# Optimization experiments

Measured on AMD Instinct MI355X. Metric: run time of the kernel, lower is better.

Reference implementation:

```python
import jax, jax.numpy as jnp
import numpy as np

V, E, U, B, L, H = 32000, 256, 1024, 64, 2048, 1024  # vocab, embed, dec_units, batch, enc_len, enc_hidden


def setup_inputs() -> dict:
    key = jax.random.key(0)
    ks = jax.random.split(key, 14)
    s = 0.02
    return {
        "x": jax.random.randint(ks[0], (B, 1), 0, V),
        "hidden": jax.random.normal(ks[1], (B, U), jnp.float32),
        "enc_output": jax.random.normal(ks[2], (B, L, H), jnp.float32),
        "emb": jax.random.normal(ks[3], (V, E), jnp.float32) * s,
        "w1": jax.random.normal(ks[4], (H, U), jnp.float32) * s,
        "b1": jnp.zeros((U,), jnp.float32),
        "w2": jax.random.normal(ks[5], (U, U), jnp.float32) * s,
        "b2": jnp.zeros((U,), jnp.float32),
        "v_w": jax.random.normal(ks[6], (U, 1), jnp.float32) * s,
        "v_b": jnp.zeros((1,), jnp.float32),
        "gru_k": jax.random.normal(ks[7], (H + E, 3 * U), jnp.float32) * s,
        "gru_rk": jax.random.normal(ks[8], (U, 3 * U), jnp.float32) * s,
        "gru_b": jnp.zeros((3 * U,), jnp.float32),
        "out_w": jax.random.normal(ks[9], (U, V), jnp.float32) * s,
        "out_b": jnp.zeros((V,), jnp.float32),
    }


def reference(x, hidden, enc_output, emb, w1, b1, w2, b2, v_w, v_b,
              gru_k, gru_rk, gru_b, out_w, out_b):
    # ---- Bahdanau additive attention ----
    # score: [B, L, 1]
    hid_t = (hidden @ w2 + b2)[:, None, :]                      # [B,1,U]
    score = jnp.tanh(enc_output @ w1 + b1 + hid_t) @ v_w + v_b  # [B,L,1]
    attention_weights = jax.nn.softmax(score, axis=1)           # softmax over seq axis
    context = jnp.sum(attention_weights * enc_output, axis=1)   # [B,H]

    # ---- embed current token and concat [context, embedded] ----
    xe = emb[x[:, 0]]                                           # [B,E]
    xin = jnp.concatenate([context, xe], axis=-1)               # [B,H+E]

    # ---- single GRU step; original calls gru(x) w/o initial_state -> h0 = 0 ----
    # Keras gate order [z, r, h], reset_after=False
    h0 = jnp.zeros((xin.shape[0], U), xin.dtype)
    zi = xin @ gru_k + gru_b                                    # [B,3U]
    z = jax.nn.sigmoid(zi[:, :U] + h0 @ gru_rk[:, :U])
    r = jax.nn.sigmoid(zi[:, U:2 * U] + h0 @ gru_rk[:, U:2 * U])
    hh = jnp.tanh(zi[:, 2 * U:] + (r * h0) @ gru_rk[:, 2 * U:])
    state = z * h0 + (1.0 - z) * hh                             # [B,U]

    # ---- output projection ----
    logits = state @ out_w + out_b                              # [B,V]
    return logits, state, attention_weights
```

## Files before the change

### kernel.cpp

```cpp
#include <hip/hip_runtime.h>
#include <hip/hip_bf16.h>
#include <stdint.h>

#define Bz 64
#define Lz 2048
#define Hz 1024
#define Uz 1024
#define Vz 32000
#define Ez 256

typedef __attribute__((ext_vector_type(8))) short bf16x8;
typedef __attribute__((ext_vector_type(4))) float f32x4;

__device__ __forceinline__ unsigned short f2bf(float f) {
    unsigned int u = __float_as_uint(f);
    u += 0x7fffu + ((u >> 16) & 1u);
    return (unsigned short)(u >> 16);
}

__device__ __forceinline__ float tanh_fast(float x) {
    float e = __expf(2.0f * x);
    return (e - 1.0f) * __builtin_amdgcn_rcpf(e + 1.0f);
}

__device__ __forceinline__ void async_cp16(const void* g, void* l) {
    __builtin_amdgcn_global_load_lds(
        (const __attribute__((address_space(1))) void*)g,
        (__attribute__((address_space(3))) void*)l, 16, 0, 0);
}

__global__ void pack_w1_kernel(const float* __restrict__ w1,
                               unsigned short* __restrict__ w1p) {
    __shared__ float tile[32][257];
    int nb = blockIdx.x;
    int kb = blockIdx.y;
    int t  = threadIdx.x;
#pragma unroll
    for (int i = 0; i < 32; ++i)
        tile[i][t] = w1[(size_t)(kb * 32 + i) * Uz + nb * 256 + t];
    __syncthreads();
    union { uint4 v[4]; unsigned short s[32]; } u;
#pragma unroll
    for (int kk = 0; kk < 32; ++kk) u.s[kk] = f2bf(tile[kk][t]);
    uint4* d4 = (uint4*)(w1p + (size_t)kb * 32768 + (size_t)(nb * 256 + t) * 32);
#pragma unroll
    for (int j = 0; j < 4; ++j) d4[j] = u.v[j];
}

__global__ void transpose_hidden_kernel(const float* __restrict__ hidden,
                                        float* __restrict__ hT) {
    __shared__ float tile[64][65];
    int cb = blockIdx.x;
    int t  = threadIdx.x;
    int tc = t & 63, tr = t >> 6;
#pragma unroll
    for (int i = 0; i < 16; ++i) {
        int r = i * 4 + tr;
        tile[r][tc] = hidden[(size_t)r * Uz + cb * 64 + tc];
    }
    __syncthreads();
#pragma unroll
    for (int i = 0; i < 16; ++i) {
        int k = i * 4 + tr;
        hT[(size_t)(cb * 64 + k) * 64 + tc] = tile[tc][k];
    }
}

__global__ __launch_bounds__(256)
void hid_gemm_kernel(const float* __restrict__ hT, const float* __restrict__ w2,
                     float* __restrict__ hid) {
    int col = blockIdx.x * 256 + threadIdx.x;
    int k0  = blockIdx.y * 64;
    float acc[64];
#pragma unroll
    for (int r = 0; r < 64; ++r) acc[r] = 0.f;
#pragma unroll 4
    for (int k = 0; k < 64; ++k) {
        float w = w2[(size_t)(k0 + k) * Uz + col];
        const float* srow = hT + (size_t)(k0 + k) * 64;
#pragma unroll
        for (int r = 0; r < 64; ++r) acc[r] = fmaf(srow[r], w, acc[r]);
    }
#pragma unroll
    for (int r = 0; r < 64; ++r) atomicAdd(&hid[(size_t)r * Uz + col], acc[r]);
}

__global__ __launch_bounds__(256, 2)
void score_kernel(const float* __restrict__ enc,
                  const unsigned short* __restrict__ w1p,
                  const float* __restrict__ b1, const float* __restrict__ b2,
                  const float* __restrict__ hid, const float* __restrict__ vw,
                  float* __restrict__ scores) {
    __shared__ __align__(16) float lA[64 * 32];
    __shared__ __align__(16) unsigned short lB[512 * 32];

    const int t    = threadIdx.x;
    const int lane = t & 63;
    const int wave = t >> 6;
    const int ln   = lane & 15;
    const int q    = lane >> 4;
    const int n0   = blockIdx.x * 512;
    const int m0   = blockIdx.y * 64;
    const int bidx = m0 >> 11;

    f32x4 acc[4][8];
    const f32x4 zero = {0.f, 0.f, 0.f, 0.f};
#pragma unroll
    for (int ms = 0; ms < 4; ++ms)
#pragma unroll
        for (int s = 0; s < 8; ++s) acc[ms][s] = zero;

    const char* w1base = ((const char*)w1p) + n0 * 64;

    for (int kt = 0; kt < 32; ++kt) {
        __syncthreads();
        const char* bsrc = w1base + kt * 65536;
#pragma unroll
        for (int i = 0; i < 8; ++i) {
            int cb = i * 256 + t;
            async_cp16(bsrc + cb * 16, ((char*)lB) + cb * 16);
        }
#pragma unroll
        for (int i = 0; i < 2; ++i) {
            int P = i * 256 + t;
            int m = P >> 3, p = P & 7;
            int c = p ^ (m & 7);
            async_cp16(enc + (size_t)(m0 + m) * Hz + kt * 32 + c * 4,
                       ((char*)lA) + P * 16);
        }
        __syncthreads();

        bf16x8 afr[4];
#pragma unroll
        for (int ms = 0; ms < 4; ++ms) {
            int m = ms * 16 + ln;
            int c0 = (2 * q) ^ (m & 7);
            int c1 = (2 * q + 1) ^ (m & 7);
            float4 x0 = *(const float4*)&lA[m * 32 + c0 * 4];
            float4 x1 = *(const float4*)&lA[m * 32 + c1 * 4];
            union { bf16x8 v; __hip_bfloat162 h[4]; } u;
            u.h[0] = __float22bfloat162_rn(make_float2(x0.x, x0.y));
            u.h[1] = __float22bfloat162_rn(make_float2(x0.z, x0.w));
            u.h[2] = __float22bfloat162_rn(make_float2(x1.x, x1.y));
            u.h[3] = __float22bfloat162_rn(make_float2(x1.z, x1.w));
            afr[ms] = u.v;
        }
#pragma unroll
        for (int s = 0; s < 8; ++s) {
            int nl = wave * 128 + s * 16 + ln;
            bf16x8 bfr = *(const bf16x8*)&lB[nl * 32 + q * 8];
#pragma unroll
            for (int ms = 0; ms < 4; ++ms)
                acc[ms][s] = __builtin_amdgcn_mfma_f32_16x16x32_bf16(
                    afr[ms], bfr, acc[ms][s], 0, 0, 0);
        }
    }

    const float* hidb = hid + bidx * Uz;
    float psum[4][4];
#pragma unroll
    for (int ms = 0; ms < 4; ++ms)
#pragma unroll
        for (int r = 0; r < 4; ++r) psum[ms][r] = 0.f;
#pragma unroll
    for (int s = 0; s < 8; ++s) {
        int n = n0 + wave * 128 + s * 16 + ln;
        float bias = b1[n] + b2[n] + hidb[n];
        float vwn = vw[n];
#pragma unroll
        for (int ms = 0; ms < 4; ++ms)
#pragma unroll
            for (int r = 0; r < 4; ++r)
                psum[ms][r] += tanh_fast(acc[ms][s][r] + bias) * vwn;
    }
#pragma unroll
    for (int ms = 0; ms < 4; ++ms)
#pragma unroll
        for (int r = 0; r < 4; ++r) {
            float v = psum[ms][r];
            v += __shfl_xor(v, 1);
            v += __shfl_xor(v, 2);
            v += __shfl_xor(v, 4);
            v += __shfl_xor(v, 8);
            if (ln == 0) atomicAdd(&scores[m0 + ms * 16 + q * 4 + r], v);
        }
}

__global__ void softmax_kernel(const float* __restrict__ scores,
                               float* __restrict__ attn) {
    int b = blockIdx.x, t = threadIdx.x;
    __shared__ float sm[4], ss[4];
    float v[8];
    float mx = -1e30f;
#pragma unroll
    for (int i = 0; i < 8; ++i) {
        v[i] = scores[b * Lz + i * 256 + t];
        mx = fmaxf(mx, v[i]);
    }
    for (int o = 1; o < 64; o <<= 1) mx = fmaxf(mx, __shfl_xor(mx, o));
    if ((t & 63) == 0) sm[t >> 6] = mx;
    __syncthreads();
    mx = fmaxf(fmaxf(sm[0], sm[1]), fmaxf(sm[2], sm[3]));
    float sum = 0.f;
#pragma unroll
    for (int i = 0; i < 8; ++i) { v[i] = __expf(v[i] - mx); sum += v[i]; }
    for (int o = 1; o < 64; o <<= 1) sum += __shfl_xor(sum, o);
    if ((t & 63) == 0) ss[t >> 6] = sum;
    __syncthreads();
    sum = ss[0] + ss[1] + ss[2] + ss[3];
    float inv = 1.0f / sum;
#pragma unroll
    for (int i = 0; i < 8; ++i) attn[b * Lz + i * 256 + t] = v[i] * inv;
}

__global__ void context_kernel(const float* __restrict__ enc,
                               const float* __restrict__ attn,
                               float* __restrict__ ctx) {
    int h  = blockIdx.x * 256 + threadIdx.x;
    int l0 = blockIdx.y * 512;
    int b  = blockIdx.z;
    const float* ep = enc + ((size_t)b * Lz + l0) * Hz + h;
    const float* ap = attn + b * Lz + l0;
    float acc = 0.f;
#pragma unroll 8
    for (int l = 0; l < 512; ++l) acc = fmaf(ap[l], ep[(size_t)l * Hz], acc);
    atomicAdd(&ctx[b * Uz + h], acc);
}

__global__ void gru_kernel(const int* __restrict__ x,
                           const float* __restrict__ emb,
                           const float* __restrict__ ctx,
                           const float* __restrict__ gk,
                           const float* __restrict__ gb,
                           float* __restrict__ state,
                           float* __restrict__ stateT) {
    int u  = blockIdx.y * 256 + threadIdx.x;
    int b0 = blockIdx.x * 2;
    float az0 = 0, az1 = 0, ah0 = 0, ah1 = 0;
    const float* c0 = ctx + b0 * Uz;
    const float* c1 = c0 + Uz;
    const float* e0 = emb + (size_t)x[b0] * Ez;
    const float* e1 = emb + (size_t)x[b0 + 1] * Ez;
    for (int k = 0; k < Hz; ++k) {
        float wz = gk[(size_t)k * 3072 + u];
        float wh = gk[(size_t)k * 3072 + 2048 + u];
        float x0 = c0[k], x1 = c1[k];
        az0 = fmaf(x0, wz, az0); ah0 = fmaf(x0, wh, ah0);
        az1 = fmaf(x1, wz, az1); ah1 = fmaf(x1, wh, ah1);
    }
    for (int k = 0; k < Ez; ++k) {
        float wz = gk[(size_t)(Hz + k) * 3072 + u];
        float wh = gk[(size_t)(Hz + k) * 3072 + 2048 + u];
        float x0 = e0[k], x1 = e1[k];
        az0 = fmaf(x0, wz, az0); ah0 = fmaf(x0, wh, ah0);
        az1 = fmaf(x1, wz, az1); ah1 = fmaf(x1, wh, ah1);
    }
    float gz = gb[u], gh = gb[2048 + u];
    float z0 = __builtin_amdgcn_rcpf(1.f + __expf(-(az0 + gz)));
    float z1 = __builtin_amdgcn_rcpf(1.f + __expf(-(az1 + gz)));
    float s0 = (1.f - z0) * tanh_fast(ah0 + gh);
    float s1 = (1.f - z1) * tanh_fast(ah1 + gh);
    state[b0 * Uz + u]       = s0;
    state[(b0 + 1) * Uz + u] = s1;
    stateT[(size_t)u * 64 + b0]     = s0;
    stateT[(size_t)u * 64 + b0 + 1] = s1;
}

__global__ __launch_bounds__(256)
void logits_kernel(const float* __restrict__ stateT,
                   const float* __restrict__ ow, const float* __restrict__ ob,
                   float* __restrict__ out) {
    int col = blockIdx.x * 256 + threadIdx.x;
    int k0  = blockIdx.y * 256;
    float acc[64];
#pragma unroll
    for (int r = 0; r < 64; ++r) acc[r] = 0.f;
#pragma unroll 4
    for (int k = 0; k < 256; ++k) {
        float w = ow[(size_t)(k0 + k) * Vz + col];
        const float* srow = stateT + (size_t)(k0 + k) * 64;
#pragma unroll
        for (int r = 0; r < 64; ++r) acc[r] = fmaf(srow[r], w, acc[r]);
    }
    float bb = (blockIdx.y == 0) ? ob[col] : 0.f;
#pragma unroll
    for (int r = 0; r < 64; ++r)
        atomicAdd(&out[(size_t)r * Vz + col], acc[r] + bb);
}

extern "C" void kernel_launch(void* const* d_in, const int* in_sizes, int n_in,
                              void* d_out, int out_size, void* d_ws, size_t ws_size,
                              hipStream_t stream) {
    const int*   x      = (const int*)d_in[0];
    const float* hidden = (const float*)d_in[1];
    const float* enc    = (const float*)d_in[2];
    const float* emb    = (const float*)d_in[3];
    const float* w1     = (const float*)d_in[4];
    const float* b1     = (const float*)d_in[5];
    const float* w2     = (const float*)d_in[6];
    const float* b2     = (const float*)d_in[7];
    const float* vw     = (const float*)d_in[8];
    const float* gk     = (const float*)d_in[10];
    const float* gb     = (const float*)d_in[12];
    const float* ow     = (const float*)d_in[13];
    const float* ob     = (const float*)d_in[14];

    float* out    = (float*)d_out;
    float* logits = out;
    float* state  = out + (size_t)Bz * Vz;
    float* attn   = state + (size_t)Bz * Uz;

    char* ws = (char*)d_ws;
    float* scores = (float*)ws;
    float* ctx    = (float*)(ws + 524288);
    float* hid    = (float*)(ws + 786432);
    unsigned short* w1p = (unsigned short*)(ws + 1048576);
    float* stateT = (float*)(ws + 3145728);
    float* hT     = (float*)(ws + 3407872);

    hipMemsetAsync(d_ws, 0, 1048576, stream);
    hipMemsetAsync(d_out, 0, (size_t)Bz * Vz * sizeof(float), stream);

    pack_w1_kernel<<<dim3(4, 32), 256, 0, stream>>>(w1, w1p);
    transpose_hidden_kernel<<<16, 256, 0, stream>>>(hidden, hT);
    hid_gemm_kernel<<<dim3(4, 16), 256, 0, stream>>>(hT, w2, hid);
    score_kernel<<<dim3(2, Bz * Lz / 64), 256, 0, stream>>>(enc, w1p, b1, b2,
                                                            hid, vw, scores);
    softmax_kernel<<<Bz, 256, 0, stream>>>(scores, attn);
    context_kernel<<<dim3(4, 4, Bz), 256, 0, stream>>>(enc, attn, ctx);
    gru_kernel<<<dim3(Bz / 2, 4), 256, 0, stream>>>(x, emb, ctx, gk, gb, state,
                                                    stateT);
    logits_kernel<<<dim3(125, 4), 256, 0, stream>>>(stateT, ow, ob, logits);
}
```

Baseline: 1.455 ms.

## Retile attention score GEMM to 128x128 with 32x32 MFMA and rework logits GEMM

The score GEMM moves from 64x512 tiles with 16x16x32 MFMA to 128x128 tiles with 32x32x16 MFMA. Each encoder tile is converted to bf16 once when staged into LDS, instead of every wave re-converting fp32 fragments, and both operands use an XOR-swizzled LDS layout. The w1 packing kernel is changed to emit matching 64-wide swizzled K blocks. The logits GEMM now gives each thread an 8x4 register tile with float4 loads and a larger K split per block. The smaller N tile means each encoder row is fetched by more blocks, which raises global and L2 traffic on the largest input.

Result: slower. 1.658 ms (+14.0%).

```diff
diff --git a/kernel.cpp b/kernel.cpp
--- a/kernel.cpp
+++ b/kernel.cpp
@@ -11,6 +11,7 @@
 
 typedef __attribute__((ext_vector_type(8))) short bf16x8;
 typedef __attribute__((ext_vector_type(4))) float f32x4;
+typedef __attribute__((ext_vector_type(16))) float f32x16;
 
 __device__ __forceinline__ unsigned short f2bf(float f) {
     unsigned int u = __float_as_uint(f);
@@ -31,20 +32,22 @@
 
 __global__ void pack_w1_kernel(const float* __restrict__ w1,
                                unsigned short* __restrict__ w1p) {
-    __shared__ float tile[32][257];
-    int nb = blockIdx.x;
-    int kb = blockIdx.y;
-    int t  = threadIdx.x;
-#pragma unroll
-    for (int i = 0; i < 32; ++i)
-        tile[i][t] = w1[(size_t)(kb * 32 + i) * Uz + nb * 256 + t];
+    __shared__ unsigned short tb[64][264];
+    int nb = blockIdx.x, kt = blockIdx.y, t = threadIdx.x;
+#pragma unroll
+    for (int i = 0; i < 64; ++i)
+        tb[i][t] = f2bf(w1[(size_t)(kt * 64 + i) * Uz + nb * 256 + t]);
     __syncthreads();
-    union { uint4 v[4]; unsigned short s[32]; } u;
-#pragma unroll
-    for (int kk = 0; kk < 32; ++kk) u.s[kk] = f2bf(tile[kk][t]);
-    uint4* d4 = (uint4*)(w1p + (size_t)kb * 32768 + (size_t)(nb * 256 + t) * 32);
-#pragma unroll
-    for (int j = 0; j < 4; ++j) d4[j] = u.v[j];
+    int n = nb * 256 + t;
+    unsigned short* dst = w1p + (size_t)kt * 65536 + (size_t)n * 64;
+#pragma unroll
+    for (int p = 0; p < 8; ++p) {
+        int c = p ^ (n & 7);
+        union { uint4 v; unsigned short s[8]; } u;
+#pragma unroll
+        for (int j = 0; j < 8; ++j) u.s[j] = tb[c * 8 + j][t];
+        *(uint4*)(dst + p * 8) = u.v;
+    }
 }
 
 __global__ void transpose_hidden_kernel(const float* __restrict__ hidden,
@@ -85,105 +88,109 @@
     for (int r = 0; r < 64; ++r) atomicAdd(&hid[(size_t)r * Uz + col], acc[r]);
 }
 
-__global__ __launch_bounds__(256, 2)
+__global__ __launch_bounds__(256, 4)
 void score_kernel(const float* __restrict__ enc,
                   const unsigned short* __restrict__ w1p,
                   const float* __restrict__ b1, const float* __restrict__ b2,
                   const float* __restrict__ hid, const float* __restrict__ vw,
                   float* __restrict__ scores) {
-    __shared__ __align__(16) float lA[64 * 32];
-    __shared__ __align__(16) unsigned short lB[512 * 32];
+    __shared__ __align__(16) unsigned short lA[128 * 64];
+    __shared__ __align__(16) unsigned short lB[128 * 64];
 
     const int t    = threadIdx.x;
     const int lane = t & 63;
     const int wave = t >> 6;
-    const int ln   = lane & 15;
-    const int q    = lane >> 4;
-    const int n0   = blockIdx.x * 512;
-    const int m0   = blockIdx.y * 64;
+    const int ln   = lane & 31;
+    const int kh   = lane >> 5;
+    const int wm   = wave & 1;
+    const int wn   = wave >> 1;
+    const int n0   = blockIdx.x * 128;
+    const int m0   = blockIdx.y * 128;
     const int bidx = m0 >> 11;
-
-    f32x4 acc[4][8];
-    const f32x4 zero = {0.f, 0.f, 0.f, 0.f};
-#pragma unroll
-    for (int ms = 0; ms < 4; ++ms)
-#pragma unroll
-        for (int s = 0; s < 8; ++s) acc[ms][s] = zero;
-
-    const char* w1base = ((const char*)w1p) + n0 * 64;
-
-    for (int kt = 0; kt < 32; ++kt) {
+    const int sw   = ln & 7;
+
+    f32x16 acc[2][2];
+#pragma unroll
+    for (int i = 0; i < 2; ++i)
+#pragma unroll
+        for (int j = 0; j < 2; ++j)
+#pragma unroll
+            for (int r = 0; r < 16; ++r) acc[i][j][r] = 0.f;
+
+    const int  mrow = t >> 3;
+    const int  ca   = (t & 7) ^ (mrow & 7);
+    const float* encb = enc + (size_t)(m0 + mrow) * Hz + ca * 8;
+    const char* w1bb = ((const char*)w1p) + (size_t)n0 * 128 + (size_t)t * 16;
+
+    const int mA0 = (wm * 64 + ln) * 128, mA1 = mA0 + 32 * 128;
+    const int nB0 = (wn * 64 + ln) * 128, nB1 = nB0 + 32 * 128;
+
+    for (int kt = 0; kt < 16; ++kt) {
         __syncthreads();
-        const char* bsrc = w1base + kt * 65536;
-#pragma unroll
-        for (int i = 0; i < 8; ++i) {
-            int cb = i * 256 + t;
-            async_cp16(bsrc + cb * 16, ((char*)lB) + cb * 16);
-        }
-#pragma unroll
-        for (int i = 0; i < 2; ++i) {
-            int P = i * 256 + t;
-            int m = P >> 3, p = P & 7;
-            int c = p ^ (m & 7);
-            async_cp16(enc + (size_t)(m0 + m) * Hz + kt * 32 + c * 4,
-                       ((char*)lA) + P * 16);
+#pragma unroll
+        for (int i = 0; i < 4; ++i)
+            async_cp16(w1bb + (size_t)kt * 131072 + i * 4096,
+                       ((char*)lB) + (i * 256 + t) * 16);
+        float4 f[8];
+#pragma unroll
+        for (int i = 0; i < 4; ++i) {
+            const float* s = encb + (size_t)i * 32 * Hz + kt * 64;
+            f[2 * i]     = *(const float4*)(s);
+            f[2 * i + 1] = *(const float4*)(s + 4);
+        }
+#pragma unroll
+        for (int i = 0; i < 4; ++i) {
+            union { uint4 u; __hip_bfloat162 h[4]; } w;
+            w.h[0] = __float22bfloat162_rn(make_float2(f[2*i].x,   f[2*i].y));
+            w.h[1] = __float22bfloat162_rn(make_float2(f[2*i].z,   f[2*i].w));
+            w.h[2] = __float22bfloat162_rn(make_float2(f[2*i+1].x, f[2*i+1].y));
+            w.h[3] = __float22bfloat162_rn(make_float2(f[2*i+1].z, f[2*i+1].w));
+            *(uint4*)(((char*)lA) + (i * 256 + t) * 16) = w.u;
         }
         __syncthreads();
-
-        bf16x8 afr[4];
-#pragma unroll
-        for (int ms = 0; ms < 4; ++ms) {
-            int m = ms * 16 + ln;
-            int c0 = (2 * q) ^ (m & 7);
-            int c1 = (2 * q + 1) ^ (m & 7);
-            float4 x0 = *(const float4*)&lA[m * 32 + c0 * 4];
-            float4 x1 = *(const float4*)&lA[m * 32 + c1 * 4];
-            union { bf16x8 v; __hip_bfloat162 h[4]; } u;
-            u.h[0] = __float22bfloat162_rn(make_float2(x0.x, x0.y));
-            u.h[1] = __float22bfloat162_rn(make_float2(x0.z, x0.w));
-            u.h[2] = __float22bfloat162_rn(make_float2(x1.x, x1.y));
-            u.h[3] = __float22bfloat162_rn(make_float2(x1.z, x1.w));
-            afr[ms] = u.v;
-        }
-#pragma unroll
-        for (int s = 0; s < 8; ++s) {
-            int nl = wave * 128 + s * 16 + ln;
-            bf16x8 bfr = *(const bf16x8*)&lB[nl * 32 + q * 8];
-#pragma unroll
-            for (int ms = 0; ms < 4; ++ms)
-                acc[ms][s] = __builtin_amdgcn_mfma_f32_16x16x32_bf16(
-                    afr[ms], bfr, acc[ms][s], 0, 0, 0);
-        }
-    }
-
-    const float* hidb = hid + bidx * Uz;
-    float psum[4][4];
-#pragma unroll
-    for (int ms = 0; ms < 4; ++ms)
-#pragma unroll
-        for (int r = 0; r < 4; ++r) psum[ms][r] = 0.f;
-#pragma unroll
-    for (int s = 0; s < 8; ++s) {
-        int n = n0 + wave * 128 + s * 16 + ln;
-        float bias = b1[n] + b2[n] + hidb[n];
-        float vwn = vw[n];
-#pragma unroll
-        for (int ms = 0; ms < 4; ++ms)
-#pragma unroll
-            for (int r = 0; r < 4; ++r)
-                psum[ms][r] += tanh_fast(acc[ms][s][r] + bias) * vwn;
-    }
-#pragma unroll
-    for (int ms = 0; ms < 4; ++ms)
-#pragma unroll
-        for (int r = 0; r < 4; ++r) {
-            float v = psum[ms][r];
+#pragma unroll
+        for (int ks = 0; ks < 4; ++ks) {
+            const int off = ((2 * ks + kh) ^ sw) * 16;
+            bf16x8 a0 = *(const bf16x8*)(((const char*)lA) + mA0 + off);
+            bf16x8 a1 = *(const bf16x8*)(((const char*)lA) + mA1 + off);
+            bf16x8 b0 = *(const bf16x8*)(((const char*)lB) + nB0 + off);
+            bf16x8 b1f = *(const bf16x8*)(((const char*)lB) + nB1 + off);
+            acc[0][0] = __builtin_amdgcn_mfma_f32_32x32x16_bf16(a0, b0,  acc[0][0], 0, 0, 0);
+            acc[0][1] = __builtin_amdgcn_mfma_f32_32x32x16_bf16(a0, b1f, acc[0][1], 0, 0, 0);
+            acc[1][0] = __builtin_amdgcn_mfma_f32_32x32x16_bf16(a1, b0,  acc[1][0], 0, 0, 0);
+            acc[1][1] = __builtin_amdgcn_mfma_f32_32x32x16_bf16(a1, b1f, acc[1][1], 0, 0, 0);
+        }
+    }
+
+    const float* hidb = hid + (size_t)bidx * Uz;
+#pragma unroll
+    for (int mt = 0; mt < 2; ++mt) {
+        float ps[16];
+#pragma unroll
+        for (int r = 0; r < 16; ++r) ps[r] = 0.f;
+#pragma unroll
+        for (int nt = 0; nt < 2; ++nt) {
+            int n = n0 + wn * 64 + nt * 32 + ln;
+            float bias = b1[n] + b2[n] + hidb[n];
+            float vwn = vw[n];
+#pragma unroll
+            for (int r = 0; r < 16; ++r)
+                ps[r] += tanh_fast(acc[mt][nt][r] + bias) * vwn;
+        }
+#pragma unroll
+        for (int r = 0; r < 16; ++r) {
+            float v = ps[r];
             v += __shfl_xor(v, 1);
             v += __shfl_xor(v, 2);
             v += __shfl_xor(v, 4);
             v += __shfl_xor(v, 8);
-            if (ln == 0) atomicAdd(&scores[m0 + ms * 16 + q * 4 + r], v);
-        }
+            v += __shfl_xor(v, 16);
+            if (ln == 0) {
+                int row = (r & 3) + 8 * (r >> 2) + 4 * kh;
+                atomicAdd(&scores[m0 + wm * 64 + mt * 32 + row], v);
+            }
+        }
+    }
 }
 
 __global__ void softmax_kernel(const float* __restrict__ scores,
@@ -270,22 +277,40 @@
 void logits_kernel(const float* __restrict__ stateT,
                    const float* __restrict__ ow, const float* __restrict__ ob,
                    float* __restrict__ out) {
-    int col = blockIdx.x * 256 + threadIdx.x;
-    int k0  = blockIdx.y * 256;
-    float acc[64];
-#pragma unroll
-    for (int r = 0; r < 64; ++r) acc[r] = 0.f;
-#pragma unroll 4
-    for (int k = 0; k < 256; ++k) {
-        float w = ow[(size_t)(k0 + k) * Vz + col];
-        const float* srow = stateT + (size_t)(k0 + k) * 64;
-#pragma unroll
-        for (int r = 0; r < 64; ++r) acc[r] = fmaf(srow[r], w, acc[r]);
-    }
-    float bb = (blockIdx.y == 0) ? ob[col] : 0.f;
-#pragma unroll
-    for (int r = 0; r < 64; ++r)
-        atomicAdd(&out[(size_t)r * Vz + col], acc[r] + bb);
+    int t  = threadIdx.x;
+    int rg = t >> 5;
+    int ct = t & 31;
+    int c4 = blockIdx.x * 128 + ct * 4;
+    int k0 = blockIdx.y * 512;
+    float acc[8][4];
+#pragma unroll
+    for (int i = 0; i < 8; ++i)
+#pragma unroll
+        for (int j = 0; j < 4; ++j) acc[i][j] = 0.f;
+    const float4* st4 = (const float4*)stateT;
+#pragma unroll 2
+    for (int k = 0; k < 512; ++k) {
+        int kk = k0 + k;
+        float4 w  = *(const float4*)(ow + (size_t)kk * Vz + c4);
+        float4 s0 = st4[kk * 16 + rg * 2];
+        float4 s1 = st4[kk * 16 + rg * 2 + 1];
+        float s[8] = {s0.x, s0.y, s0.z, s0.w, s1.x, s1.y, s1.z, s1.w};
+        float wv[4] = {w.x, w.y, w.z, w.w};
+#pragma unroll
+        for (int i = 0; i < 8; ++i)
+#pragma unroll
+            for (int j = 0; j < 4; ++j)
+                acc[i][j] = fmaf(s[i], wv[j], acc[i][j]);
+    }
+#pragma unroll
+    for (int i = 0; i < 8; ++i) {
+        size_t rowo = (size_t)(rg * 8 + i) * Vz + c4;
+#pragma unroll
+        for (int j = 0; j < 4; ++j) {
+            float v = acc[i][j] + ((k0 == 0) ? ob[c4 + j] : 0.f);
+            atomicAdd(&out[rowo + j], v);
+        }
+    }
 }
 
 extern "C" void kernel_launch(void* const* d_in, const int* in_sizes, int n_in,
@@ -321,14 +346,14 @@
     hipMemsetAsync(d_ws, 0, 1048576, stream);
     hipMemsetAsync(d_out, 0, (size_t)Bz * Vz * sizeof(float), stream);
 
-    pack_w1_kernel<<<dim3(4, 32), 256, 0, stream>>>(w1, w1p);
+    pack_w1_kernel<<<dim3(4, 16), 256, 0, stream>>>(w1, w1p);
     transpose_hidden_kernel<<<16, 256, 0, stream>>>(hidden, hT);
     hid_gemm_kernel<<<dim3(4, 16), 256, 0, stream>>>(hT, w2, hid);
-    score_kernel<<<dim3(2, Bz * Lz / 64), 256, 0, stream>>>(enc, w1p, b1, b2,
-                                                            hid, vw, scores);
+    score_kernel<<<dim3(8, 1024), 256, 0, stream>>>(enc, w1p, b1, b2,
+                                                    hid, vw, scores);
     softmax_kernel<<<Bz, 256, 0, stream>>>(scores, attn);
     context_kernel<<<dim3(4, 4, Bz), 256, 0, stream>>>(enc, attn, ctx);
     gru_kernel<<<dim3(Bz / 2, 4), 256, 0, stream>>>(x, emb, ctx, gk, gb, state,
                                                     stateT);
-    logits_kernel<<<dim3(125, 4), 256, 0, stream>>>(stateT, ow, ob, logits);
-}
+    logits_kernel<<<dim3(250, 2), 256, 0, stream>>>(stateT, ow, ob, logits);
+}
```
